# Kernel optimization log

Measured on AMD Instinct MI355X. Metric: run time of the kernel, lower is better.

Reference implementation:

```python
import jax, jax.numpy as jnp
import numpy as np

N, E, IN, OUT, G = 100000, 800000, 64, 64, 250


def setup_inputs() -> dict:
    key = jax.random.key(0)
    ks = jax.random.split(key, 8)
    x = jax.random.normal(ks[0], (N, IN), dtype=jnp.float32)
    edge_index = jax.random.randint(ks[1], (2, E), 0, N, dtype=jnp.int32)
    edge_weight = jax.random.uniform(ks[2], (E,), dtype=jnp.float32)
    segment_ids = jnp.sort(jax.random.randint(ks[3], (N,), 0, G, dtype=jnp.int32))
    # GCNConv parameters (glorot-ish weights, zero bias as in PyG init)
    W_embed = jax.random.normal(ks[4], (IN, OUT), dtype=jnp.float32) / np.sqrt(IN)
    b_embed = jnp.zeros((OUT,), dtype=jnp.float32)
    W_pool = jax.random.normal(ks[5], (IN, 1), dtype=jnp.float32) / np.sqrt(IN)
    b_pool = jnp.zeros((1,), dtype=jnp.float32)
    return dict(x=x, W_embed=W_embed, b_embed=b_embed, W_pool=W_pool,
                b_pool=b_pool, edge_weight=edge_weight, edge_index=edge_index,
                segment_ids=segment_ids, num_segments=G)


def _gcn(x, W, b, row, col, ew, n):
    """PyG GCNConv: symmetric norm with self-loops already appended."""
    h = x @ W                                            # [N, F]
    deg = jax.ops.segment_sum(ew, col, num_segments=n)   # in-degree incl. self-loops
    dinv = jnp.where(deg > 0, jax.lax.rsqrt(deg), 0.0)
    norm = dinv[row] * ew * dinv[col]                    # [E+N]
    out = jax.ops.segment_sum(norm[:, None] * h[row], col, num_segments=n)
    return out + b


def reference(x, W_embed, b_embed, W_pool, b_pool, edge_weight,
              edge_index, segment_ids, num_segments):
    n = x.shape[0]
    loop = jnp.arange(n, dtype=edge_index.dtype)
    row = jnp.concatenate([edge_index[0], loop])         # add self-loops (w=1)
    col = jnp.concatenate([edge_index[1], loop])
    ew = jnp.concatenate([edge_weight, jnp.ones((n,), edge_weight.dtype)])

    embed = jax.nn.relu(_gcn(x, W_embed, b_embed, row, col, ew, n))  # [N, OUT]
    score = _gcn(x, W_pool, b_pool, row, col, ew, n)[:, 0]           # [N]

    # ragged per-graph softmax over node scores (stable)
    m = jax.ops.segment_max(score, segment_ids, num_segments=num_segments)
    e = jnp.exp(score - m[segment_ids])
    z = jax.ops.segment_sum(e, segment_ids, num_segments=num_segments)
    s = e / z[segment_ids]                               # [N]

    # softmax-weighted pooling of embeddings per graph -> [G, OUT]
    res = jax.ops.segment_sum(s[:, None] * embed, segment_ids,
                              num_segments=num_segments)
    return res
```

## Files before the change

### kernel.cpp

```cpp
#include <hip/hip_runtime.h>
#include <math.h>

#define NIN 64
#define CAP 16
#define GSEG 250
#define POOL_SPLIT 8
#define BND 128
#define BSH 7
#define CHUNK 2048
#define NBMAX 1024
#define OVRMAX 256
#define TS 17

__device__ __forceinline__ float wave_reduce_sum(float v) {
    #pragma unroll
    for (int off = 32; off > 0; off >>= 1) v += __shfl_xor(v, off);
    return v;
}

__device__ __forceinline__ unsigned short f2bf(float f) {
    unsigned int u = __float_as_uint(f);
    u += 0x7FFFu + ((u >> 16) & 1u);
    return (unsigned short)(u >> 16);
}
__device__ __forceinline__ float bf2f(unsigned short h) {
    return __uint_as_float(((unsigned int)h) << 16);
}
__device__ __forceinline__ float bflo(unsigned int u) { return __uint_as_float(u << 16); }
__device__ __forceinline__ float bfhi(unsigned int u) { return __uint_as_float(u & 0xFFFF0000u); }
__device__ __forceinline__ unsigned int pack2bf(float lo, float hi) {
    return (unsigned int)f2bf(lo) | ((unsigned int)f2bf(hi) << 16);
}

__device__ __forceinline__ unsigned int f15enc(float w) {
    unsigned int u = __float_as_uint(w);
    u += 0x0FFFu + ((u >> 13) & 1u);
    int e5 = (int)(u >> 23) - 96;
    if (e5 <= 0) return 0u;
    unsigned int m = (u >> 13) & 0x3FFu;
    if (e5 > 31) { e5 = 31; m = 0x3FFu; }
    return ((unsigned int)e5 << 10) | m;
}
__device__ __forceinline__ float f15dec(unsigned int f) {
    if (f == 0u) return 0.0f;
    return __uint_as_float((((f >> 10) + 96u) << 23) | ((f & 0x3FFu) << 13));
}

__device__ __forceinline__ int wave_excl_scan_int(int x, int lane) {
    int inc = x;
    #pragma unroll
    for (int off = 1; off < 64; off <<= 1) {
        int y = __shfl_up(inc, off);
        if (lane >= off) inc += y;
    }
    return inc - x;
}

__device__ __forceinline__ void scan_btot(const int* __restrict__ src,
                                          int* dst, int nb, int tid) {
    if (tid < 64) {
        int v[16];
        #pragma unroll
        for (int j = 0; j < 16; ++j) {
            int idx = tid * 16 + j;
            v[j] = (idx < nb) ? src[idx] : 0;
        }
        int loc = 0;
        #pragma unroll
        for (int j = 0; j < 16; ++j) loc += v[j];
        int ex = wave_excl_scan_int(loc, tid);
        int run = ex;
        #pragma unroll
        for (int j = 0; j < 16; ++j) {
            int idx = tid * 16 + j;
            if (idx < nb) { dst[idx] = run; run += v[j]; }
        }
    }
}

__global__ void __launch_bounds__(256)
k_prep(ushort4* __restrict__ x164, const float4* __restrict__ x4,
       float* __restrict__ out, int* __restrict__ gstart, int* __restrict__ gend,
       const int* __restrict__ col, int* __restrict__ ghist,
       int n, int e, int nb, int nblk) {
    __shared__ int h[NBMAX];
    int tid = threadIdx.x, blk = blockIdx.x;
    int i = blk * 256 + tid;
    int tot = n * (NIN / 4);
    if (i < tot) {
        float4 v = x4[i];
        ushort4 hh;
        hh.x = f2bf(v.x); hh.y = f2bf(v.y); hh.z = f2bf(v.z); hh.w = f2bf(v.w);
        x164[i] = hh;
    }
    if (i < GSEG * NIN) out[i] = 0.0f;
    if (i < GSEG) { gstart[i] = 0; gend[i] = 0; }
    if (blk < nblk) {
        for (int j = tid; j < NBMAX; j += 256) h[j] = 0;
        __syncthreads();
        int base = blk * CHUNK;
        int end = base + CHUNK; if (end > e) end = e;
        for (int j = base + tid; j < end; j += 256) atomicAdd(&h[col[j] >> BSH], 1);
        __syncthreads();
        for (int b = tid; b < nb; b += 256) ghist[blk * nb + b] = h[b];
    }
}

__global__ void __launch_bounds__(256)
k_scanA(int* __restrict__ ghist, int* __restrict__ btot,
        const int* __restrict__ seg, int* __restrict__ gstart,
        int* __restrict__ gend, int nblk, int nb, int n) {
    int tid = threadIdx.x;
    int b = blockIdx.x;
    if (tid < 64) {
        int lane = tid;
        int v[8];
        #pragma unroll
        for (int j = 0; j < 8; ++j) {
            int idx = lane * 8 + j;
            v[j] = (idx < nblk) ? ghist[idx * nb + b] : 0;
        }
        int loc = 0;
        #pragma unroll
        for (int j = 0; j < 8; ++j) loc += v[j];
        int ex = wave_excl_scan_int(loc, lane);
        int run = ex;
        #pragma unroll
        for (int j = 0; j < 8; ++j) {
            int idx = lane * 8 + j;
            if (idx < nblk) { int t = v[j]; ghist[idx * nb + b] = run; run += t; }
        }
        if (lane == 63) btot[b] = ex + loc;
    }
    int gsz = gridDim.x * 256;
    for (int i = b * 256 + tid; i < n; i += gsz) {
        int s = seg[i];
        if (i == 0 || seg[i - 1] != s) gstart[s] = i;
        if (i == n - 1 || seg[i + 1] != s) gend[s] = i + 1;
    }
}

__global__ void __launch_bounds__(256)
k_scatter(const int* __restrict__ row, const int* __restrict__ col,
          const float* __restrict__ ew, const int* __restrict__ ghist,
          const int* __restrict__ btot, uint2* __restrict__ bins,
          int e, int nb) {
    __shared__ int h[NBMAX];
    __shared__ int loff[NBMAX];
    __shared__ int gdst[NBMAX];
    __shared__ int bb[NBMAX];
    __shared__ uint2 recs[CHUNK];
    __shared__ unsigned short rb[CHUNK];
    int tid = threadIdx.x, blk = blockIdx.x;
    int base = blk * CHUNK;
    int end = base + CHUNK; if (end > e) end = e;
    int cntc = end - base;

    for (int i = tid; i < NBMAX; i += 256) h[i] = 0;
    __syncthreads();
    for (int i = base + tid; i < end; i += 256) atomicAdd(&h[col[i] >> BSH], 1);
    __syncthreads();
    if (tid < 64) {
        int v[16];
        #pragma unroll
        for (int j = 0; j < 16; ++j) {
            int idx = tid * 16 + j;
            v[j] = (idx < nb) ? h[idx] : 0;
        }
        int loc = 0;
        #pragma unroll
        for (int j = 0; j < 16; ++j) loc += v[j];
        int ex = wave_excl_scan_int(loc, tid);
        int run = ex;
        #pragma unroll
        for (int j = 0; j < 16; ++j) {
            int idx = tid * 16 + j;
            if (idx < nb) { loff[idx] = run; run += v[j]; }
        }
    }
    scan_btot(btot, bb, nb, tid);
    __syncthreads();
    for (int b = tid; b < nb; b += 256) gdst[b] = bb[b] + ghist[blk * nb + b];
    for (int i = tid; i < NBMAX; i += 256) h[i] = 0;
    __syncthreads();
    for (int i = base + tid; i < end; i += 256) {
        int c = col[i], r = row[i];
        int b = c >> BSH;
        uint2 rec;
        rec.x = (unsigned int)r;
        rec.y = ((unsigned int)(c & (BND - 1)) << 15) | f15enc(ew[i]);
        int k = atomicAdd(&h[b], 1);
        int idx = loff[b] + k;
        recs[idx] = rec;
        rb[idx] = (unsigned short)b;
    }
    __syncthreads();
    for (int i = tid; i < cntc; i += 256) {
        int b = rb[i];
        bins[(size_t)gdst[b] + (i - loff[b])] = recs[i];
    }
}

__global__ void __launch_bounds__(256)
k_deg2(const uint2* __restrict__ bins, const int* __restrict__ btot,
       float* __restrict__ dinv, int n, int nb) {
    __shared__ float sdeg[BND];
    __shared__ int bb[NBMAX];
    int tid = threadIdx.x;
    int b = blockIdx.x;
    int c0 = b << BSH;
    if (tid < BND) sdeg[tid] = 0.0f;
    scan_btot(btot, bb, nb, tid);
    __syncthreads();
    int s0 = bb[b], tot = btot[b];
    for (int i = tid; i < tot; i += 256) {
        uint2 rec = bins[(size_t)s0 + i];
        int cl = (int)((rec.y >> 15) & (BND - 1));
        atomicAdd(&sdeg[cl], f15dec(rec.y & 0x7FFFu));
    }
    __syncthreads();
    if (tid < BND && c0 + tid < n) dinv[c0 + tid] = rsqrtf(sdeg[tid] + 1.0f);
}

__global__ void __launch_bounds__(256)
k_bg(const uint2* __restrict__ bins, const int* __restrict__ btot,
     const float* __restrict__ dinv, const ushort* __restrict__ x16,
     ushort* __restrict__ agg16, const float* __restrict__ Wp,
     const float* __restrict__ bp, float* __restrict__ score, int n, int nb) {
    __shared__ unsigned int rows[BND * TS];
    __shared__ float wts[BND * TS];
    __shared__ float sdv[BND];
    __shared__ int scnt[BND];
    __shared__ int bb[NBMAX];
    __shared__ int ovr_cl[OVRMAX];
    __shared__ int ovr_r[OVRMAX];
    __shared__ float ovr_w[OVRMAX];
    __shared__ int ovn;
    int tid = threadIdx.x;
    int b = blockIdx.x;
    int c0 = b << BSH;

    if (tid < BND) {
        scnt[tid] = 0;
        int c = c0 + tid;
        sdv[tid] = dinv[c < n ? c : (n - 1)];
    }
    if (tid == 0) ovn = 0;
    scan_btot(btot, bb, nb, tid);
    __syncthreads();

    int s0 = bb[b], tot = btot[b];
    for (int i = tid; i < tot; i += 256) {
        uint2 rec = bins[(size_t)s0 + i];
        int cl = (int)((rec.y >> 15) & (BND - 1));
        int r = (int)rec.x;
        float w = f15dec(rec.y & 0x7FFFu) * dinv[r] * sdv[cl];
        int slot = atomicAdd(&scnt[cl], 1);
        if (slot < CAP) {
            rows[cl * TS + slot] = (unsigned int)r;
            wts[cl * TS + slot] = w;
        } else {
            int oi = atomicAdd(&ovn, 1);
            if (oi < OVRMAX) { ovr_cl[oi] = cl; ovr_r[oi] = r; ovr_w[oi] = w; }
        }
    }
    __syncthreads();

    int lane = tid & 63, wv = tid >> 6;
    int o = lane >> 3, l = lane & 7;
    const float4* wp4 = (const float4*)Wp;
    float4 w0 = wp4[2 * l], w1 = wp4[2 * l + 1];
    float bp0 = bp[0];
    const uint4* xr4 = (const uint4*)x16;
    int nov = ovn;

    #pragma unroll
    for (int it = 0; it < BND / 32; ++it) {
        int bl = it * 32 + wv * 8;
        int nl = bl + o;
        int c = c0 + nl;
        bool valid = c < n;
        int cc = valid ? c : (n - 1);
        int cr = scnt[nl];
        int m = valid ? (cr < CAP ? cr : CAP) : 0;
        float di = sdv[nl];

        int pr0 = (int)rows[nl * TS + 2 * l];
        float pw0 = wts[nl * TS + 2 * l];
        int pr1 = (int)rows[nl * TS + 2 * l + 1];
        float pw1 = wts[nl * TS + 2 * l + 1];

        uint4 xs = xr4[(size_t)cc * 8 + l];
        float s2 = di * di;
        float a0 = s2 * bflo(xs.x), a1 = s2 * bfhi(xs.x);
        float a2 = s2 * bflo(xs.y), a3 = s2 * bfhi(xs.y);
        float a4 = s2 * bflo(xs.z), a5 = s2 * bfhi(xs.z);
        float a6 = s2 * bflo(xs.w), a7 = s2 * bfhi(xs.w);

        int base = lane & 56;
        #pragma unroll
        for (int k = 0; k < 8; ++k) {
            int rk = __shfl((k & 1) ? pr1 : pr0, base + (k >> 1));
            float wk = __shfl((k & 1) ? pw1 : pw0, base + (k >> 1));
            bool v = k < m;
            int r = v ? rk : 0;
            float w = v ? wk : 0.0f;
            uint4 xr = xr4[(size_t)r * 8 + l];
            a0 = fmaf(w, bflo(xr.x), a0); a1 = fmaf(w, bfhi(xr.x), a1);
            a2 = fmaf(w, bflo(xr.y), a2); a3 = fmaf(w, bfhi(xr.y), a3);
            a4 = fmaf(w, bflo(xr.z), a4); a5 = fmaf(w, bfhi(xr.z), a5);
            a6 = fmaf(w, bflo(xr.w), a6); a7 = fmaf(w, bfhi(xr.w), a7);
        }
        if (__any(m > 8)) {
            #pragma unroll
            for (int k = 8; k < CAP; ++k) {
                int rk = __shfl((k & 1) ? pr1 : pr0, base + (k >> 1));
                float wk = __shfl((k & 1) ? pw1 : pw0, base + (k >> 1));
                bool v = k < m;
                int r = v ? rk : 0;
                float w = v ? wk : 0.0f;
                uint4 xr = xr4[(size_t)r * 8 + l];
                a0 = fmaf(w, bflo(xr.x), a0); a1 = fmaf(w, bfhi(xr.x), a1);
                a2 = fmaf(w, bflo(xr.y), a2); a3 = fmaf(w, bfhi(xr.y), a3);
                a4 = fmaf(w, bflo(xr.z), a4); a5 = fmaf(w, bfhi(xr.z), a5);
                a6 = fmaf(w, bflo(xr.w), a6); a7 = fmaf(w, bfhi(xr.w), a7);
            }
        }
        for (int i = 0; i < nov; ++i) {
            int cl = ovr_cl[i];
            if (cl >= bl && cl < bl + 8) {
                int r = ovr_r[i];
                float wm = (cl == nl) ? ovr_w[i] : 0.0f;
                uint4 xr = xr4[(size_t)r * 8 + l];
                a0 = fmaf(wm, bflo(xr.x), a0); a1 = fmaf(wm, bfhi(xr.x), a1);
                a2 = fmaf(wm, bflo(xr.y), a2); a3 = fmaf(wm, bfhi(xr.y), a3);
                a4 = fmaf(wm, bflo(xr.z), a4); a5 = fmaf(wm, bfhi(xr.z), a5);
                a6 = fmaf(wm, bflo(xr.w), a6); a7 = fmaf(wm, bfhi(xr.w), a7);
            }
        }

        if (valid) {
            uint4 ho;
            ho.x = pack2bf(a0, a1); ho.y = pack2bf(a2, a3);
            ho.z = pack2bf(a4, a5); ho.w = pack2bf(a6, a7);
            ((uint4*)agg16)[(size_t)cc * 8 + l] = ho;
        }
        float part = a0 * w0.x + a1 * w0.y + a2 * w0.z + a3 * w0.w
                   + a4 * w1.x + a5 * w1.y + a6 * w1.z + a7 * w1.w;
        part += __shfl_xor(part, 1);
        part += __shfl_xor(part, 2);
        part += __shfl_xor(part, 4);
        if (l == 0 && valid) score[c] = part + bp0;
    }
}

#define WLOAD(i) float4 wq##i = make_float4(We[(4*(i)+0)*NIN+lane], We[(4*(i)+1)*NIN+lane], \
                                            We[(4*(i)+2)*NIN+lane], We[(4*(i)+3)*NIN+lane]);
#define WSTEP(i) { float4 av = *(const float4*)&als[wv][4*(i)]; \
    e0 = fmaf(av.x, wq##i.x, e0); e1 = fmaf(av.y, wq##i.y, e1); \
    e2 = fmaf(av.z, wq##i.z, e2); e3 = fmaf(av.w, wq##i.w, e3); }

__global__ void __launch_bounds__(256)
k_pool(const ushort* __restrict__ agg16, const float* __restrict__ score,
       const float* __restrict__ We, const float* __restrict__ be,
       const int* __restrict__ gstart, const int* __restrict__ gend,
       float* __restrict__ out) {
    int g = blockIdx.x / POOL_SPLIT;
    int p = blockIdx.x % POOL_SPLIT;
    int tid = threadIdx.x;
    int wv = tid >> 6, lane = tid & 63;
    int s = gstart[g], e = gend[g];

    __shared__ float red[4];
    __shared__ float bc;

    float mx = -3.402823466e38f;
    for (int i = s + tid; i < e; i += 256) mx = fmaxf(mx, score[i]);
    #pragma unroll
    for (int off = 32; off > 0; off >>= 1) mx = fmaxf(mx, __shfl_xor(mx, off));
    if (lane == 0) red[wv] = mx;
    __syncthreads();
    if (tid == 0) bc = fmaxf(fmaxf(red[0], red[1]), fmaxf(red[2], red[3]));
    __syncthreads();
    float m = bc;
    __syncthreads();

    float sm = 0.0f;
    for (int i = s + tid; i < e; i += 256) sm += __expf(score[i] - m);
    sm = wave_reduce_sum(sm);
    if (lane == 0) red[wv] = sm;
    __syncthreads();
    if (tid == 0) bc = red[0] + red[1] + red[2] + red[3];
    __syncthreads();
    float invz = (bc > 0.0f) ? 1.0f / bc : 0.0f;

    WLOAD(0) WLOAD(1) WLOAD(2) WLOAD(3) WLOAD(4) WLOAD(5) WLOAD(6) WLOAD(7)
    WLOAD(8) WLOAD(9) WLOAD(10) WLOAD(11) WLOAD(12) WLOAD(13) WLOAD(14) WLOAD(15)
    float bj = be[lane];

    __shared__ float als[4][NIN];
    __shared__ float part[4][NIN];

    const int stride = POOL_SPLIT * 4;
    int n = s + p * 4 + wv;
    float acc = 0.0f;

    float a_cur = 0.0f, sw_cur = 0.0f;
    if (n < e) {
        a_cur = bf2f(agg16[(size_t)n * NIN + lane]);
        sw_cur = __expf(score[n] - m) * invz;
    }
    while (n < e) {
        int nn = n + stride;
        bool vn = nn < e;
        int ni = vn ? nn : n;
        float a_nxt = bf2f(agg16[(size_t)ni * NIN + lane]);
        float sw_nxt = __expf(score[ni] - m) * invz;

        als[wv][lane] = a_cur;
        float e0 = bj, e1 = 0.0f, e2 = 0.0f, e3 = 0.0f;
        WSTEP(0) WSTEP(1) WSTEP(2) WSTEP(3) WSTEP(4) WSTEP(5) WSTEP(6) WSTEP(7)
        WSTEP(8) WSTEP(9) WSTEP(10) WSTEP(11) WSTEP(12) WSTEP(13) WSTEP(14) WSTEP(15)
        float emb = fmaxf(e0 + e1 + e2 + e3, 0.0f);
        acc = fmaf(sw_cur, emb, acc);

        a_cur = a_nxt; sw_cur = sw_nxt;
        n = nn;
    }
    part[wv][lane] = acc;
    __syncthreads();
    if (wv == 0) {
        float r = part[0][lane] + part[1][lane] + part[2][lane] + part[3][lane];
        atomicAdd(&out[(size_t)g * NIN + lane], r);
    }
}

extern "C" void kernel_launch(void* const* d_in, const int* in_sizes, int n_in,
                              void* d_out, int out_size, void* d_ws, size_t ws_size,
                              hipStream_t stream) {
    const float* x  = (const float*)d_in[0];
    const float* We = (const float*)d_in[1];
    const float* be = (const float*)d_in[2];
    const float* Wp = (const float*)d_in[3];
    const float* bp = (const float*)d_in[4];
    const float* ew = (const float*)d_in[5];
    const int* eidx = (const int*)d_in[6];
    const int* seg  = (const int*)d_in[7];

    int N = in_sizes[0] / NIN;
    int E = in_sizes[5];
    const int* row = eidx;
    const int* col = eidx + E;
    int nb   = (N + BND - 1) / BND;
    int nblk = (E + CHUNK - 1) / CHUNK;

    char* w = (char*)d_ws;
    auto alloc = [&](size_t bytes) {
        char* p = w;
        w += (bytes + 255) & ~(size_t)255;
        return p;
    };
    unsigned short* x16    = (unsigned short*)alloc((size_t)N * NIN * sizeof(short));
    unsigned short* agg16  = (unsigned short*)alloc((size_t)N * NIN * sizeof(short));
    float*          dinv   = (float*)alloc((size_t)N * sizeof(float));
    uint2*          bins   = (uint2*)alloc((size_t)E * sizeof(uint2));
    int*            ghist  = (int*)  alloc((size_t)nblk * nb * sizeof(int));
    int*            btot   = (int*)  alloc((size_t)nb * sizeof(int));
    float*          score  = (float*)alloc((size_t)N * sizeof(float));
    int*            gstart = (int*)  alloc(GSEG * sizeof(int));
    int*            gend   = (int*)  alloc(GSEG * sizeof(int));
    float* out = (float*)d_out;

    int b = 256;
    int g_prep = (N * (NIN / 4) + b - 1) / b;

    k_prep<<<g_prep, b, 0, stream>>>((ushort4*)x16, (const float4*)x, out, gstart,
                                     gend, col, ghist, N, E, nb, nblk);
    k_scanA<<<nb, b, 0, stream>>>(ghist, btot, seg, gstart, gend, nblk, nb, N);
    k_scatter<<<nblk, b, 0, stream>>>(row, col, ew, ghist, btot, bins, E, nb);
    k_deg2<<<nb, b, 0, stream>>>(bins, btot, dinv, N, nb);
    k_bg<<<nb, b, 0, stream>>>(bins, btot, dinv, x16, agg16, Wp, bp, score, N, nb);
    k_pool<<<GSEG * POOL_SPLIT, b, 0, stream>>>(agg16, score, We, be, gstart, gend, out);
}
```

Baseline: 93.68 us.

## Split bin-gather kernel into ELL build and finely parallel gather

The fused bin-and-gather kernel becomes two kernels. One builds a per-node ELL table of (row, weight) pairs plus a per-bucket overflow list in global memory. The other gathers with one 8-lane group per node across many more small blocks, which raises parallelism and occupancy over the old one-block-per-128-nodes design. The scatter chunk size is also halved, with the scan widened to match. The cost is an extra launch and extra global traffic to write and re-read the ELL table.

```diff
diff --git a/kernel.cpp b/kernel.cpp
--- a/kernel.cpp
+++ b/kernel.cpp
@@ -7,10 +7,9 @@
 #define POOL_SPLIT 8
 #define BND 128
 #define BSH 7
-#define CHUNK 2048
+#define CHUNK 1024
 #define NBMAX 1024
-#define OVRMAX 256
-#define TS 17
+#define OVR 128
 
 __device__ __forceinline__ float wave_reduce_sum(float v) {
     #pragma unroll
@@ -114,20 +113,20 @@
     int b = blockIdx.x;
     if (tid < 64) {
         int lane = tid;
-        int v[8];
-        #pragma unroll
-        for (int j = 0; j < 8; ++j) {
-            int idx = lane * 8 + j;
+        int v[16];
+        #pragma unroll
+        for (int j = 0; j < 16; ++j) {
+            int idx = lane * 16 + j;
             v[j] = (idx < nblk) ? ghist[idx * nb + b] : 0;
         }
         int loc = 0;
         #pragma unroll
-        for (int j = 0; j < 8; ++j) loc += v[j];
+        for (int j = 0; j < 16; ++j) loc += v[j];
         int ex = wave_excl_scan_int(loc, lane);
         int run = ex;
         #pragma unroll
-        for (int j = 0; j < 8; ++j) {
-            int idx = lane * 8 + j;
+        for (int j = 0; j < 16; ++j) {
+            int idx = lane * 16 + j;
             if (idx < nblk) { int t = v[j]; ghist[idx * nb + b] = run; run += t; }
         }
         if (lane == 63) btot[b] = ex + loc;
@@ -223,19 +222,16 @@
 }
 
 __global__ void __launch_bounds__(256)
-k_bg(const uint2* __restrict__ bins, const int* __restrict__ btot,
-     const float* __restrict__ dinv, const ushort* __restrict__ x16,
-     ushort* __restrict__ agg16, const float* __restrict__ Wp,
-     const float* __restrict__ bp, float* __restrict__ score, int n, int nb) {
-    __shared__ unsigned int rows[BND * TS];
-    __shared__ float wts[BND * TS];
+k_build(const uint2* __restrict__ bins, const int* __restrict__ btot,
+        const float* __restrict__ dinv, int2* __restrict__ ell2,
+        int* __restrict__ cnt, int* __restrict__ ovfc, int2* __restrict__ ovfe,
+        int n, int nb) {
+    __shared__ int2 tile[BND * CAP];
     __shared__ float sdv[BND];
     __shared__ int scnt[BND];
     __shared__ int bb[NBMAX];
-    __shared__ int ovr_cl[OVRMAX];
-    __shared__ int ovr_r[OVRMAX];
-    __shared__ float ovr_w[OVRMAX];
-    __shared__ int ovn;
+    __shared__ int2 sovf[OVR];
+    __shared__ int sovn;
     int tid = threadIdx.x;
     int b = blockIdx.x;
     int c0 = b << BSH;
@@ -245,7 +241,7 @@
         int c = c0 + tid;
         sdv[tid] = dinv[c < n ? c : (n - 1)];
     }
-    if (tid == 0) ovn = 0;
+    if (tid == 0) sovn = 0;
     scan_btot(btot, bb, nb, tid);
     __syncthreads();
 
@@ -257,49 +253,69 @@
         float w = f15dec(rec.y & 0x7FFFu) * dinv[r] * sdv[cl];
         int slot = atomicAdd(&scnt[cl], 1);
         if (slot < CAP) {
-            rows[cl * TS + slot] = (unsigned int)r;
-            wts[cl * TS + slot] = w;
+            tile[cl * CAP + slot] = make_int2(r, __float_as_int(w));
         } else {
-            int oi = atomicAdd(&ovn, 1);
-            if (oi < OVRMAX) { ovr_cl[oi] = cl; ovr_r[oi] = r; ovr_w[oi] = w; }
-        }
-    }
-    __syncthreads();
-
+            int oi = atomicAdd(&sovn, 1);
+            if (oi < OVR) sovf[oi] = make_int2((r << BSH) | cl, __float_as_int(w));
+        }
+    }
+    __syncthreads();
+    int nn = n - c0; if (nn > BND) nn = BND;
+    for (int i = tid; i < nn * CAP; i += 256)
+        ell2[(size_t)c0 * CAP + i] = tile[i];
+    if (tid < nn) cnt[c0 + tid] = scnt[tid];
+    int nov = sovn < OVR ? sovn : OVR;
+    if (tid == 0) ovfc[b] = nov;
+    for (int i = tid; i < nov; i += 256) ovfe[(size_t)b * OVR + i] = sovf[i];
+}
+
+__global__ void __launch_bounds__(256)
+k_gather(const ushort* __restrict__ x16, const float* __restrict__ dinv,
+         const int* __restrict__ cnt, const int2* __restrict__ ell2,
+         const int* __restrict__ ovfc, const int2* __restrict__ ovfe,
+         ushort* __restrict__ agg16, const float* __restrict__ Wp,
+         const float* __restrict__ bp, float* __restrict__ score, int n) {
+    int tid = threadIdx.x, blk = blockIdx.x;
     int lane = tid & 63, wv = tid >> 6;
     int o = lane >> 3, l = lane & 7;
-    const float4* wp4 = (const float4*)Wp;
-    float4 w0 = wp4[2 * l], w1 = wp4[2 * l + 1];
-    float bp0 = bp[0];
+    int c = blk * 32 + wv * 8 + o;
+    bool valid = c < n;
+    int cc = valid ? c : (n - 1);
+    int b = blk >> 2;
+
+    int cr = cnt[cc];
+    int m = valid ? (cr < CAP ? cr : CAP) : 0;
+    float di = dinv[cc];
+
+    uint4 pe = ((const uint4*)ell2)[(size_t)cc * 8 + l];
+    int pr0 = (int)pe.x; float pw0 = __uint_as_float(pe.y);
+    int pr1 = (int)pe.z; float pw1 = __uint_as_float(pe.w);
+
     const uint4* xr4 = (const uint4*)x16;
-    int nov = ovn;
-
+    uint4 xs = xr4[(size_t)cc * 8 + l];
+    float s2 = di * di;
+    float a0 = s2 * bflo(xs.x), a1 = s2 * bfhi(xs.x);
+    float a2 = s2 * bflo(xs.y), a3 = s2 * bfhi(xs.y);
+    float a4 = s2 * bflo(xs.z), a5 = s2 * bfhi(xs.z);
+    float a6 = s2 * bflo(xs.w), a7 = s2 * bfhi(xs.w);
+
+    int base = lane & 56;
     #pragma unroll
-    for (int it = 0; it < BND / 32; ++it) {
-        int bl = it * 32 + wv * 8;
-        int nl = bl + o;
-        int c = c0 + nl;
-        bool valid = c < n;
-        int cc = valid ? c : (n - 1);
-        int cr = scnt[nl];
-        int m = valid ? (cr < CAP ? cr : CAP) : 0;
-        float di = sdv[nl];
-
-        int pr0 = (int)rows[nl * TS + 2 * l];
-        float pw0 = wts[nl * TS + 2 * l];
-        int pr1 = (int)rows[nl * TS + 2 * l + 1];
-        float pw1 = wts[nl * TS + 2 * l + 1];
-
-        uint4 xs = xr4[(size_t)cc * 8 + l];
-        float s2 = di * di;
-        float a0 = s2 * bflo(xs.x), a1 = s2 * bfhi(xs.x);
-        float a2 = s2 * bflo(xs.y), a3 = s2 * bfhi(xs.y);
-        float a4 = s2 * bflo(xs.z), a5 = s2 * bfhi(xs.z);
-        float a6 = s2 * bflo(xs.w), a7 = s2 * bfhi(xs.w);
-
-        int base = lane & 56;
-        #pragma unroll
-        for (int k = 0; k < 8; ++k) {
+    for (int k = 0; k < 8; ++k) {
+        int rk = __shfl((k & 1) ? pr1 : pr0, base + (k >> 1));
+        float wk = __shfl((k & 1) ? pw1 : pw0, base + (k >> 1));
+        bool v = k < m;
+        int r = v ? rk : 0;
+        float w = v ? wk : 0.0f;
+        uint4 xr = xr4[(size_t)r * 8 + l];
+        a0 = fmaf(w, bflo(xr.x), a0); a1 = fmaf(w, bfhi(xr.x), a1);
+        a2 = fmaf(w, bflo(xr.y), a2); a3 = fmaf(w, bfhi(xr.y), a3);
+        a4 = fmaf(w, bflo(xr.z), a4); a5 = fmaf(w, bfhi(xr.z), a5);
+        a6 = fmaf(w, bflo(xr.w), a6); a7 = fmaf(w, bfhi(xr.w), a7);
+    }
+    if (__any(m > 8)) {
+        #pragma unroll
+        for (int k = 8; k < CAP; ++k) {
             int rk = __shfl((k & 1) ? pr1 : pr0, base + (k >> 1));
             float wk = __shfl((k & 1) ? pw1 : pw0, base + (k >> 1));
             bool v = k < m;
@@ -311,47 +327,34 @@
             a4 = fmaf(w, bflo(xr.z), a4); a5 = fmaf(w, bfhi(xr.z), a5);
             a6 = fmaf(w, bflo(xr.w), a6); a7 = fmaf(w, bfhi(xr.w), a7);
         }
-        if (__any(m > 8)) {
-            #pragma unroll
-            for (int k = 8; k < CAP; ++k) {
-                int rk = __shfl((k & 1) ? pr1 : pr0, base + (k >> 1));
-                float wk = __shfl((k & 1) ? pw1 : pw0, base + (k >> 1));
-                bool v = k < m;
-                int r = v ? rk : 0;
-                float w = v ? wk : 0.0f;
-                uint4 xr = xr4[(size_t)r * 8 + l];
-                a0 = fmaf(w, bflo(xr.x), a0); a1 = fmaf(w, bfhi(xr.x), a1);
-                a2 = fmaf(w, bflo(xr.y), a2); a3 = fmaf(w, bfhi(xr.y), a3);
-                a4 = fmaf(w, bflo(xr.z), a4); a5 = fmaf(w, bfhi(xr.z), a5);
-                a6 = fmaf(w, bflo(xr.w), a6); a7 = fmaf(w, bfhi(xr.w), a7);
-            }
-        }
-        for (int i = 0; i < nov; ++i) {
-            int cl = ovr_cl[i];
-            if (cl >= bl && cl < bl + 8) {
-                int r = ovr_r[i];
-                float wm = (cl == nl) ? ovr_w[i] : 0.0f;
-                uint4 xr = xr4[(size_t)r * 8 + l];
-                a0 = fmaf(wm, bflo(xr.x), a0); a1 = fmaf(wm, bfhi(xr.x), a1);
-                a2 = fmaf(wm, bflo(xr.y), a2); a3 = fmaf(wm, bfhi(xr.y), a3);
-                a4 = fmaf(wm, bflo(xr.z), a4); a5 = fmaf(wm, bfhi(xr.z), a5);
-                a6 = fmaf(wm, bflo(xr.w), a6); a7 = fmaf(wm, bfhi(xr.w), a7);
-            }
-        }
-
-        if (valid) {
-            uint4 ho;
-            ho.x = pack2bf(a0, a1); ho.y = pack2bf(a2, a3);
-            ho.z = pack2bf(a4, a5); ho.w = pack2bf(a6, a7);
-            ((uint4*)agg16)[(size_t)cc * 8 + l] = ho;
-        }
-        float part = a0 * w0.x + a1 * w0.y + a2 * w0.z + a3 * w0.w
-                   + a4 * w1.x + a5 * w1.y + a6 * w1.z + a7 * w1.w;
-        part += __shfl_xor(part, 1);
-        part += __shfl_xor(part, 2);
-        part += __shfl_xor(part, 4);
-        if (l == 0 && valid) score[c] = part + bp0;
-    }
+    }
+    int novb = ovfc[b];
+    for (int i = 0; i < novb; ++i) {
+        int2 ent = ovfe[(size_t)b * OVR + i];
+        int cl = ent.x & (BND - 1);
+        int r = ent.x >> BSH;
+        float wm = ((b << BSH) + cl == cc && valid) ? __int_as_float(ent.y) : 0.0f;
+        uint4 xr = xr4[(size_t)r * 8 + l];
+        a0 = fmaf(wm, bflo(xr.x), a0); a1 = fmaf(wm, bfhi(xr.x), a1);
+        a2 = fmaf(wm, bflo(xr.y), a2); a3 = fmaf(wm, bfhi(xr.y), a3);
+        a4 = fmaf(wm, bflo(xr.z), a4); a5 = fmaf(wm, bfhi(xr.z), a5);
+        a6 = fmaf(wm, bflo(xr.w), a6); a7 = fmaf(wm, bfhi(xr.w), a7);
+    }
+
+    if (valid) {
+        uint4 ho;
+        ho.x = pack2bf(a0, a1); ho.y = pack2bf(a2, a3);
+        ho.z = pack2bf(a4, a5); ho.w = pack2bf(a6, a7);
+        ((uint4*)agg16)[(size_t)cc * 8 + l] = ho;
+    }
+    const float4* wp4 = (const float4*)Wp;
+    float4 w0 = wp4[2 * l], w1 = wp4[2 * l + 1];
+    float part = a0 * w0.x + a1 * w0.y + a2 * w0.z + a3 * w0.w
+               + a4 * w1.x + a5 * w1.y + a6 * w1.z + a7 * w1.w;
+    part += __shfl_xor(part, 1);
+    part += __shfl_xor(part, 2);
+    part += __shfl_xor(part, 4);
+    if (l == 0 && valid) score[c] = part + bp[0];
 }
 
 #define WLOAD(i) float4 wq##i = make_float4(We[(4*(i)+0)*NIN+lane], We[(4*(i)+1)*NIN+lane], \
@@ -463,22 +466,29 @@
     unsigned short* x16    = (unsigned short*)alloc((size_t)N * NIN * sizeof(short));
     unsigned short* agg16  = (unsigned short*)alloc((size_t)N * NIN * sizeof(short));
     float*          dinv   = (float*)alloc((size_t)N * sizeof(float));
+    int*            cnt    = (int*)  alloc((size_t)N * sizeof(int));
     uint2*          bins   = (uint2*)alloc((size_t)E * sizeof(uint2));
+    int2*           ell2   = (int2*) alloc((size_t)N * CAP * sizeof(int2));
     int*            ghist  = (int*)  alloc((size_t)nblk * nb * sizeof(int));
     int*            btot   = (int*)  alloc((size_t)nb * sizeof(int));
+    int*            ovfc   = (int*)  alloc((size_t)nb * sizeof(int));
+    int2*           ovfe   = (int2*) alloc((size_t)nb * OVR * sizeof(int2));
     float*          score  = (float*)alloc((size_t)N * sizeof(float));
     int*            gstart = (int*)  alloc(GSEG * sizeof(int));
     int*            gend   = (int*)  alloc(GSEG * sizeof(int));
     float* out = (float*)d_out;
 
     int b = 256;
-    int g_prep = (N * (NIN / 4) + b - 1) / b;
+    int g_prep   = (N * (NIN / 4) + b - 1) / b;
+    int g_gather = (N + 31) / 32;
 
     k_prep<<<g_prep, b, 0, stream>>>((ushort4*)x16, (const float4*)x, out, gstart,
                                      gend, col, ghist, N, E, nb, nblk);
     k_scanA<<<nb, b, 0, stream>>>(ghist, btot, seg, gstart, gend, nblk, nb, N);
     k_scatter<<<nblk, b, 0, stream>>>(row, col, ew, ghist, btot, bins, E, nb);
     k_deg2<<<nb, b, 0, stream>>>(bins, btot, dinv, N, nb);
-    k_bg<<<nb, b, 0, stream>>>(bins, btot, dinv, x16, agg16, Wp, bp, score, N, nb);
+    k_build<<<nb, b, 0, stream>>>(bins, btot, dinv, ell2, cnt, ovfc, ovfe, N, nb);
+    k_gather<<<g_gather, b, 0, stream>>>(x16, dinv, cnt, ell2, ovfc, ovfe,
+                                         agg16, Wp, bp, score, N);
     k_pool<<<GSEG * POOL_SPLIT, b, 0, stream>>>(agg16, score, We, be, gstart, gend, out);
 }
```

After: 100.5 us. 1.07x slower.
